# Performance work log

Hardware: AMD Instinct MI355X
Metric: run time of the kernel (lower is better)

The kernel has to match this reference:

```python
import jax, jax.numpy as jnp
import numpy as np

B, Hh, Ww, C = 4, 64, 64, 64


def setup_inputs() -> dict:
    key = jax.random.key(0)
    ks = jax.random.split(key, 5)
    scale = 1.0 / np.sqrt(C)
    return {
        "x": jax.random.normal(ks[0], (B, Hh, Ww, C), dtype=jnp.float32),
        "Wq": jax.random.normal(ks[1], (C, C), dtype=jnp.float32) * scale,
        "bq": jnp.zeros((C,), dtype=jnp.float32),
        "Wk": jax.random.normal(ks[2], (C, C), dtype=jnp.float32) * scale,
        "bk": jnp.zeros((C,), dtype=jnp.float32),
        "Wv": jax.random.normal(ks[3], (C, C), dtype=jnp.float32) * scale,
        "bv": jnp.zeros((C,), dtype=jnp.float32),
        "gamma": jax.random.normal(ks[4], (1,), dtype=jnp.float32) * 0.05,
    }


def reference(x, Wq, bq, Wk, bk, Wv, bv, gamma):
    b, h, w, c = x.shape
    n = h * w
    # 1x1 convs == per-pixel dense projections
    q = (jnp.einsum('bhwc,cf->bhwf', x, Wq) + bq).reshape(b, n, c)
    k = (jnp.einsum('bhwc,cf->bhwf', x, Wk) + bk).reshape(b, n, c)
    v = (jnp.einsum('bhwc,cf->bhwf', x, Wv) + bv).reshape(b, n, c)
    # energy[b, i, j] = <q_i, k_j>; no scaling, softmax over last axis (j)
    energy = jnp.einsum('bic,bjc->bij', q, k)
    attn = jax.nn.softmax(energy, axis=-1)
    # original: transpose(matmul(value^T, attention)) -> out[b,n,c] = sum_m attn[b,m,n] * v[b,m,c]
    out = jnp.einsum('bmn,bmc->bnc', attn, v)
    out = out.reshape(b, h, w, c)
    return gamma * out + x
```

## Files before the change

### kernel.cpp

```cpp
#include <hip/hip_runtime.h>
#include <hip/hip_bf16.h>


typedef __attribute__((ext_vector_type(8))) short short8;
typedef __attribute__((ext_vector_type(4))) short short4b;
typedef __attribute__((ext_vector_type(4))) float f32x4;
typedef __attribute__((ext_vector_type(4))) unsigned int u32x4;
typedef __attribute__((ext_vector_type(2))) unsigned int u32x2;

#define DEV static __device__ __forceinline__
#define LOG2E 1.4426950408889634f

DEV unsigned short f2bf(float f) {
    __hip_bfloat16 h = __float2bfloat16(f);
    return __builtin_bit_cast(unsigned short, h);
}
DEV unsigned int pack2(float lo, float hi) {
    return (unsigned int)f2bf(lo) | ((unsigned int)f2bf(hi) << 16);
}
DEV f32x4 MFMA32(short8 a, short8 b, f32x4 c) {
    return __builtin_amdgcn_mfma_f32_16x16x32_bf16(a, b, c, 0, 0, 0);
}
DEV f32x4 MFMA16(short4b a, short4b b, f32x4 c) {
#if __has_builtin(__builtin_amdgcn_mfma_f32_16x16x16_bf16)
    return __builtin_amdgcn_mfma_f32_16x16x16_bf16(a, b, c, 0, 0, 0);
#elif __has_builtin(__builtin_amdgcn_mfma_f32_16x16x16bf16_1k)
    return __builtin_amdgcn_mfma_f32_16x16x16bf16_1k(a, b, c, 0, 0, 0);
#else
    f32x4 d = c;
    asm volatile("v_mfma_f32_16x16x16_bf16 %0, %1, %2, %0" : "+v"(d) : "v"(a), "v"(b));
    return d;
#endif
}
DEV float EXP2(float x) {
#if __has_builtin(__builtin_amdgcn_exp2f)
    return __builtin_amdgcn_exp2f(x);
#else
    return exp2f(x);
#endif
}

#define OFF_Q    0u
#define OFF_K    2097152u
#define OFF_VT   4194304u
#define OFF_WT   6291456u
#define OFF_S    6316032u
#define OFF_LR   6381568u

__global__ __launch_bounds__(256) void k0z(const float* __restrict__ Wq,
                                           const float* __restrict__ Wk,
                                           const float* __restrict__ Wv,
                                           unsigned short* __restrict__ wt,
                                           float* __restrict__ sbuf) {
    int e = blockIdx.x * 256 + threadIdx.x;
    sbuf[e] = 0.0f;
    if (e < 3 * 4096) {
        int w3 = e >> 12, rem = e & 4095, f = rem >> 6, c = rem & 63;
        const float* W = (w3 == 0) ? Wq : (w3 == 1) ? Wk : Wv;
        float s = (w3 == 0) ? LOG2E : 1.0f;
        wt[e] = f2bf(W[c * 64 + f] * s);
    }
}

__global__ __launch_bounds__(256) void k1_proj(const float* __restrict__ x,
                                               const unsigned short* __restrict__ wt,
                                               const float* __restrict__ bq,
                                               const float* __restrict__ bk,
                                               const float* __restrict__ bv,
                                               unsigned short* __restrict__ qg,
                                               unsigned short* __restrict__ kg,
                                               unsigned short* __restrict__ vtg) {
    __shared__ __align__(16) char XT[8192];
    __shared__ __align__(16) char WT1[8192];
    __shared__ __align__(16) char VTILE[9216];
    int t = threadIdx.x, blk = blockIdx.x;
    int w3 = blk >> 8, rb = blk & 255;

    {
        int m = t >> 2, q4 = t & 3;
        const f32x4* xs = (const f32x4*)(x + (size_t)(rb * 64 + m) * 64 + q4 * 16);
        f32x4 fa = xs[0], f2 = xs[1], fc = xs[2], fd = xs[3];
        u32x4 u0 = { pack2(fa[0],fa[1]), pack2(fa[2],fa[3]), pack2(f2[0],f2[1]), pack2(f2[2],f2[3]) };
        u32x4 u1 = { pack2(fc[0],fc[1]), pack2(fc[2],fc[3]), pack2(fd[0],fd[1]), pack2(fd[2],fd[3]) };
        int sw = (m & 7) << 4;
        *(u32x4*)(XT + m * 128 + ((q4 * 32) ^ sw)) = u0;
        *(u32x4*)(XT + m * 128 + ((q4 * 32 + 16) ^ sw)) = u1;
    }
    {
        int f = t >> 2, q4 = t & 3;
        const u32x4* s = (const u32x4*)(wt + w3 * 4096 + f * 64 + q4 * 16);
        u32x4 u0 = s[0], u1 = s[1];
        int sw = (f & 7) << 4;
        *(u32x4*)(WT1 + f * 128 + ((q4 * 32) ^ sw)) = u0;
        *(u32x4*)(WT1 + f * 128 + ((q4 * 32 + 16) ^ sw)) = u1;
    }
    __syncthreads();

    int lane = t & 63, wid = t >> 6, g = lane >> 4, ln = lane & 15;
    int arow = wid * 16 + ln;
    short8 a0 = *(const short8*)(XT + arow * 128 + ((16 * g) ^ ((arow & 7) << 4)));
    short8 a1 = *(const short8*)(XT + arow * 128 + ((64 + 16 * g) ^ ((arow & 7) << 4)));
    const float* bias = (w3 == 0) ? bq : (w3 == 1) ? bk : bv;
    float bscale = (w3 == 0) ? LOG2E : 1.0f;

    #pragma unroll
    for (int fb = 0; fb < 4; ++fb) {
        int frow = fb * 16 + ln;
        short8 b0 = *(const short8*)(WT1 + frow * 128 + ((16 * g) ^ ((frow & 7) << 4)));
        short8 b1 = *(const short8*)(WT1 + frow * 128 + ((64 + 16 * g) ^ ((frow & 7) << 4)));
        f32x4 acc = {0.f, 0.f, 0.f, 0.f};
        acc = MFMA32(a0, b0, acc);
        acc = MFMA32(a1, b1, acc);
        float bval = bias[frow] * bscale;
        if (w3 < 2) {
            unsigned short* dst = (w3 == 0) ? qg : kg;
            int gr = rb * 64 + wid * 16 + 4 * g;
            #pragma unroll
            for (int r = 0; r < 4; ++r)
                dst[(size_t)(gr + r) * 64 + frow] = f2bf(acc[r] + bval);
        } else {
            unsigned short* vt = (unsigned short*)VTILE;
            int mloc = wid * 16 + 4 * g;
            #pragma unroll
            for (int r = 0; r < 4; ++r)
                vt[frow * 72 + mloc + r] = f2bf(acc[r] + bval);
        }
    }
    if (w3 == 2) {
        __syncthreads();
        int f = t >> 2, mq = t & 3;
        u32x4 u0 = *(const u32x4*)(VTILE + f * 144 + mq * 32);
        u32x4 u1 = *(const u32x4*)(VTILE + f * 144 + mq * 32 + 16);
        int b = rb >> 6, n0 = (rb & 63) * 64;
        unsigned short* dst = vtg + (size_t)b * 262144 + f * 4096 + n0 + mq * 16;
        *(u32x4*)(dst) = u0;
        *(u32x4*)(dst + 8) = u1;
    }
}

__global__ __launch_bounds__(256, 8) void k2_rowsum(const unsigned short* __restrict__ qg,
                                                    const unsigned short* __restrict__ kg,
                                                    float* __restrict__ sbuf) {
    __shared__ __align__(16) char QT[8192];
    __shared__ __align__(16) char KT2[2][4096];
    int t = threadIdx.x, blk = blockIdx.x;
    int b = blk >> 9, ns = (blk >> 6) & 7, mb = blk & 63;
    int m0 = mb * 64, nbase = ns * 512;

    {
        int row = t >> 2, q4 = t & 3, sw = (row & 7) << 4;
        const u32x4* s = (const u32x4*)(qg + (size_t)(b * 4096 + m0 + row) * 64 + q4 * 16);
        u32x4 u0 = s[0], u1 = s[1];
        *(u32x4*)(QT + row * 128 + ((q4 * 32) ^ sw)) = u0;
        *(u32x4*)(QT + row * 128 + ((q4 * 32 + 16) ^ sw)) = u1;
    }
    int srow = t >> 3, sb = t & 7, ssw = (srow & 7) << 4;
    const unsigned short* kbase = kg + (size_t)(b * 4096 + nbase) * 64;
    {
        u32x4 u = *(const u32x4*)(kbase + srow * 64 + sb * 8);
        *(u32x4*)(KT2[0] + srow * 128 + ((sb * 16) ^ ssw)) = u;
    }
    __syncthreads();

    int lane = t & 63, wid = t >> 6, g = lane >> 4, ln = lane & 15;
    int arow = wid * 16 + ln;
    short8 a0 = *(const short8*)(QT + arow * 128 + ((16 * g) ^ ((arow & 7) << 4)));
    short8 a1 = *(const short8*)(QT + arow * 128 + ((64 + 16 * g) ^ ((arow & 7) << 4)));

    float acc0 = 0.f, acc1 = 0.f, acc2 = 0.f, acc3 = 0.f;
    int buf = 0;
    u32x4 pf;
    for (int nc = 0; nc < 16; ++nc) {
        if (nc < 15)
            pf = *(const u32x4*)(kbase + (size_t)((nc + 1) * 32 + srow) * 64 + sb * 8);
        const char* kt = KT2[buf];
        #pragma unroll
        for (int j = 0; j < 2; ++j) {
            int brow = j * 16 + ln, bsw = (brow & 7) << 4;
            short8 kb0 = *(const short8*)(kt + brow * 128 + ((16 * g) ^ bsw));
            short8 kb1 = *(const short8*)(kt + brow * 128 + ((64 + 16 * g) ^ bsw));
            f32x4 e = {0.f, 0.f, 0.f, 0.f};
            e = MFMA32(a0, kb0, e);
            e = MFMA32(a1, kb1, e);
            acc0 += EXP2(e[0]); acc1 += EXP2(e[1]);
            acc2 += EXP2(e[2]); acc3 += EXP2(e[3]);
        }
        if (nc < 15)
            *(u32x4*)(KT2[buf ^ 1] + srow * 128 + ((sb * 16) ^ ssw)) = pf;
        __syncthreads();
        buf ^= 1;
    }
    #pragma unroll
    for (int msk = 1; msk < 16; msk <<= 1) {
        acc0 += __shfl_xor(acc0, msk);
        acc1 += __shfl_xor(acc1, msk);
        acc2 += __shfl_xor(acc2, msk);
        acc3 += __shfl_xor(acc3, msk);
    }
    if (ln == 0) {
        float* base = sbuf + b * 4096 + m0 + wid * 16 + 4 * g;
        unsafeAtomicAdd(base + 0, acc0);
        unsafeAtomicAdd(base + 1, acc1);
        unsafeAtomicAdd(base + 2, acc2);
        unsafeAtomicAdd(base + 3, acc3);
    }
}

__global__ __launch_bounds__(256) void r2_init(const float* __restrict__ sbuf,
                                               float* __restrict__ lrbuf,
                                               const float* __restrict__ x,
                                               float* __restrict__ outp) {
    int tid = blockIdx.x * 256 + threadIdx.x;
    if (tid < 16384) lrbuf[tid] = -__log2f(sbuf[tid]);
    f32x4 v = *(const f32x4*)(x + 4 * (size_t)tid);
    *(f32x4*)(outp + 4 * (size_t)tid) = v;
}

__global__ __launch_bounds__(256, 8) void k3_out(const unsigned short* __restrict__ qg,
                                                 const unsigned short* __restrict__ kg,
                                                 const unsigned short* __restrict__ vtg,
                                                 const float* __restrict__ lrbuf,
                                                 const float* __restrict__ gamma,
                                                 float* __restrict__ outp) {
    __shared__ __align__(16) char KT[8192];
    __shared__ __align__(16) char QT2[2][2048];
    __shared__ __align__(16) char VT2[2][2560];
    int t = threadIdx.x, blk = blockIdx.x;
    int b = blk >> 9, ms = (blk >> 6) & 7, nb = blk & 63;
    int n0 = nb * 64, mbase = ms * 512;

    {
        int row = t >> 2, q4 = t & 3, sw = (row & 7) << 4;
        const u32x4* s = (const u32x4*)(kg + (size_t)(b * 4096 + n0 + row) * 64 + q4 * 16);
        u32x4 u0 = s[0], u1 = s[1];
        *(u32x4*)(KT + row * 128 + ((q4 * 32) ^ sw)) = u0;
        *(u32x4*)(KT + row * 128 + ((q4 * 32 + 16) ^ sw)) = u1;
    }
    int qrow = t >> 4, qh = t & 15;
    int vc = t >> 2, vq = t & 3;
    int qssw = (qrow & 7) << 4;
    const unsigned short* qbase = qg + (size_t)(b * 4096 + mbase) * 64;
    const unsigned short* vbase = vtg + (size_t)b * 262144 + (size_t)vc * 4096 + mbase;
    {
        u32x2 qu = *(const u32x2*)(qbase + qrow * 64 + qh * 4);
        *(u32x2*)(QT2[0] + qrow * 128 + ((qh * 8) ^ qssw)) = qu;
        u32x2 vu = *(const u32x2*)(vbase + vq * 4);
        *(u32x2*)(VT2[0] + vc * 40 + vq * 8) = vu;
    }
    int lane = t & 63, wid = t >> 6, g = lane >> 4, ln = lane & 15;
    const float* lrb = lrbuf + b * 4096 + mbase + 4 * g;
    f32x4 lcur = *(const f32x4*)(lrb);
    __syncthreads();

    int krow = wid * 16 + ln, ksw = (krow & 7) << 4;
    short8 kb0 = *(const short8*)(KT + krow * 128 + ((16 * g) ^ ksw));
    short8 kb1 = *(const short8*)(KT + krow * 128 + ((64 + 16 * g) ^ ksw));

    f32x4 z = {0.f, 0.f, 0.f, 0.f};
    f32x4 oacc[4] = {z, z, z, z};
    int qsw = (ln & 7) << 4;
    int buf = 0;
    u32x2 qpf, vpf;
    f32x4 lnext;

    for (int mc = 0; mc < 32; ++mc) {
        if (mc < 31) {
            qpf = *(const u32x2*)(qbase + (size_t)((mc + 1) * 16 + qrow) * 64 + qh * 4);
            vpf = *(const u32x2*)(vbase + (mc + 1) * 16 + vq * 4);
            lnext = *(const f32x4*)(lrb + (mc + 1) * 16);
        }
        const char* qt = QT2[buf];
        const char* vt = VT2[buf];
        short8 as0 = *(const short8*)(qt + ln * 128 + ((16 * g) ^ qsw));
        short8 as1 = *(const short8*)(qt + ln * 128 + ((64 + 16 * g) ^ qsw));
        f32x4 e = MFMA32(as1, kb1, MFMA32(as0, kb0, lcur));
        float p0 = EXP2(e[0]), p1 = EXP2(e[1]), p2 = EXP2(e[2]), p3 = EXP2(e[3]);
        u32x2 pw = { pack2(p0, p1), pack2(p2, p3) };
        short4b pa = __builtin_bit_cast(short4b, pw);
        #pragma unroll
        for (int fb = 0; fb < 4; ++fb) {
            short4b vb = *(const short4b*)(vt + (fb * 16 + ln) * 40 + g * 8);
            oacc[fb] = MFMA16(pa, vb, oacc[fb]);
        }
        if (mc < 31) {
            *(u32x2*)(QT2[buf ^ 1] + qrow * 128 + ((qh * 8) ^ qssw)) = qpf;
            *(u32x2*)(VT2[buf ^ 1] + vc * 40 + vq * 8) = vpf;
            lcur = lnext;
        }
        __syncthreads();
        buf ^= 1;
    }

    float gm = gamma[0];
    int nr = b * 4096 + n0 + wid * 16 + 4 * g;
    #pragma unroll
    for (int fb = 0; fb < 4; ++fb) {
        #pragma unroll
        for (int r = 0; r < 4; ++r)
            unsafeAtomicAdd(outp + (size_t)(nr + r) * 64 + fb * 16 + ln, gm * oacc[fb][r]);
    }
}

extern "C" void kernel_launch(void* const* d_in, const int* in_sizes, int n_in,
                              void* d_out, int out_size, void* d_ws, size_t ws_size,
                              hipStream_t stream) {
    const float* x  = (const float*)d_in[0];
    const float* Wq = (const float*)d_in[1];
    const float* bq = (const float*)d_in[2];
    const float* Wk = (const float*)d_in[3];
    const float* bk = (const float*)d_in[4];
    const float* Wv = (const float*)d_in[5];
    const float* bv = (const float*)d_in[6];
    const float* gm = (const float*)d_in[7];
    char* ws = (char*)d_ws;
    float* outp = (float*)d_out;

    unsigned short* qg  = (unsigned short*)(ws + OFF_Q);
    unsigned short* kg  = (unsigned short*)(ws + OFF_K);
    unsigned short* vtg = (unsigned short*)(ws + OFF_VT);
    unsigned short* wt  = (unsigned short*)(ws + OFF_WT);
    float* sbuf         = (float*)(ws + OFF_S);
    float* lrbuf        = (float*)(ws + OFF_LR);

    k0z<<<64, 256, 0, stream>>>(Wq, Wk, Wv, wt, sbuf);
    k1_proj<<<768, 256, 0, stream>>>(x, wt, bq, bk, bv, qg, kg, vtg);
    k2_rowsum<<<2048, 256, 0, stream>>>(qg, kg, sbuf);
    r2_init<<<1024, 256, 0, stream>>>(sbuf, lrbuf, x, outp);
    k3_out<<<2048, 256, 0, stream>>>(qg, kg, vtg, lrbuf, gm, outp);
}
```

Measured before the change: 141.2 us.

## Load MFMA operands directly from global memory, dropping LDS staging and barriers

Both the rowsum and output kernels stop staging Q, K and V tiles in shared memory. Each lane now loads its MFMA fragments straight from global memory into registers, with register double-buffering and no __syncthreads in the loop. The output kernel also swaps bf16 round-to-nearest packing for plain truncation and lowers its launch_bounds occupancy hint from 8 to 6. This removes LDS traffic and barrier stalls, but relies on L1/L2 to serve the redundant per-wave loads and loses some precision in the attention weights.

```diff
diff --git a/kernel.cpp b/kernel.cpp
--- a/kernel.cpp
+++ b/kernel.cpp
@@ -17,6 +17,11 @@
 }
 DEV unsigned int pack2(float lo, float hi) {
     return (unsigned int)f2bf(lo) | ((unsigned int)f2bf(hi) << 16);
+}
+DEV unsigned int pack2t(float lo, float hi) {
+    unsigned int ul = __builtin_bit_cast(unsigned int, lo);
+    unsigned int uh = __builtin_bit_cast(unsigned int, hi);
+    return (uh & 0xffff0000u) | (ul >> 16);
 }
 DEV f32x4 MFMA32(short8 a, short8 b, f32x4 c) {
     return __builtin_amdgcn_mfma_f32_16x16x32_bf16(a, b, c, 0, 0, 0);
@@ -141,54 +146,32 @@
 __global__ __launch_bounds__(256, 8) void k2_rowsum(const unsigned short* __restrict__ qg,
                                                     const unsigned short* __restrict__ kg,
                                                     float* __restrict__ sbuf) {
-    __shared__ __align__(16) char QT[8192];
-    __shared__ __align__(16) char KT2[2][4096];
     int t = threadIdx.x, blk = blockIdx.x;
     int b = blk >> 9, ns = (blk >> 6) & 7, mb = blk & 63;
     int m0 = mb * 64, nbase = ns * 512;
-
-    {
-        int row = t >> 2, q4 = t & 3, sw = (row & 7) << 4;
-        const u32x4* s = (const u32x4*)(qg + (size_t)(b * 4096 + m0 + row) * 64 + q4 * 16);
-        u32x4 u0 = s[0], u1 = s[1];
-        *(u32x4*)(QT + row * 128 + ((q4 * 32) ^ sw)) = u0;
-        *(u32x4*)(QT + row * 128 + ((q4 * 32 + 16) ^ sw)) = u1;
-    }
-    int srow = t >> 3, sb = t & 7, ssw = (srow & 7) << 4;
-    const unsigned short* kbase = kg + (size_t)(b * 4096 + nbase) * 64;
-    {
-        u32x4 u = *(const u32x4*)(kbase + srow * 64 + sb * 8);
-        *(u32x4*)(KT2[0] + srow * 128 + ((sb * 16) ^ ssw)) = u;
-    }
-    __syncthreads();
-
     int lane = t & 63, wid = t >> 6, g = lane >> 4, ln = lane & 15;
-    int arow = wid * 16 + ln;
-    short8 a0 = *(const short8*)(QT + arow * 128 + ((16 * g) ^ ((arow & 7) << 4)));
-    short8 a1 = *(const short8*)(QT + arow * 128 + ((64 + 16 * g) ^ ((arow & 7) << 4)));
+
+    const unsigned short* qr = qg + (size_t)(b * 4096 + m0 + wid * 16 + ln) * 64;
+    short8 a0 = *(const short8*)(qr + 8 * g);
+    short8 a1 = *(const short8*)(qr + 32 + 8 * g);
+
+    const unsigned short* kbase = kg + (size_t)(b * 4096 + nbase + ln) * 64 + 8 * g;
+    short8 kb0 = *(const short8*)(kbase);
+    short8 kb1 = *(const short8*)(kbase + 32);
 
     float acc0 = 0.f, acc1 = 0.f, acc2 = 0.f, acc3 = 0.f;
-    int buf = 0;
-    u32x4 pf;
-    for (int nc = 0; nc < 16; ++nc) {
-        if (nc < 15)
-            pf = *(const u32x4*)(kbase + (size_t)((nc + 1) * 32 + srow) * 64 + sb * 8);
-        const char* kt = KT2[buf];
-        #pragma unroll
-        for (int j = 0; j < 2; ++j) {
-            int brow = j * 16 + ln, bsw = (brow & 7) << 4;
-            short8 kb0 = *(const short8*)(kt + brow * 128 + ((16 * g) ^ bsw));
-            short8 kb1 = *(const short8*)(kt + brow * 128 + ((64 + 16 * g) ^ bsw));
-            f32x4 e = {0.f, 0.f, 0.f, 0.f};
-            e = MFMA32(a0, kb0, e);
-            e = MFMA32(a1, kb1, e);
-            acc0 += EXP2(e[0]); acc1 += EXP2(e[1]);
-            acc2 += EXP2(e[2]); acc3 += EXP2(e[3]);
+    for (int s = 0; s < 32; ++s) {
+        short8 nb0, nb1;
+        if (s < 31) {
+            const unsigned short* kp = kbase + (size_t)(s + 1) * 16 * 64;
+            nb0 = *(const short8*)(kp);
+            nb1 = *(const short8*)(kp + 32);
         }
-        if (nc < 15)
-            *(u32x4*)(KT2[buf ^ 1] + srow * 128 + ((sb * 16) ^ ssw)) = pf;
-        __syncthreads();
-        buf ^= 1;
+        f32x4 z = {0.f, 0.f, 0.f, 0.f};
+        f32x4 e = MFMA32(a1, kb1, MFMA32(a0, kb0, z));
+        acc0 += EXP2(e[0]); acc1 += EXP2(e[1]);
+        acc2 += EXP2(e[2]); acc3 += EXP2(e[3]);
+        kb0 = nb0; kb1 = nb1;
     }
     #pragma unroll
     for (int msk = 1; msk < 16; msk <<= 1) {
@@ -216,79 +199,63 @@
     *(f32x4*)(outp + 4 * (size_t)tid) = v;
 }
 
-__global__ __launch_bounds__(256, 8) void k3_out(const unsigned short* __restrict__ qg,
+__global__ __launch_bounds__(256, 6) void k3_out(const unsigned short* __restrict__ qg,
                                                  const unsigned short* __restrict__ kg,
                                                  const unsigned short* __restrict__ vtg,
                                                  const float* __restrict__ lrbuf,
                                                  const float* __restrict__ gamma,
                                                  float* __restrict__ outp) {
-    __shared__ __align__(16) char KT[8192];
-    __shared__ __align__(16) char QT2[2][2048];
-    __shared__ __align__(16) char VT2[2][2560];
     int t = threadIdx.x, blk = blockIdx.x;
     int b = blk >> 9, ms = (blk >> 6) & 7, nb = blk & 63;
     int n0 = nb * 64, mbase = ms * 512;
-
-    {
-        int row = t >> 2, q4 = t & 3, sw = (row & 7) << 4;
-        const u32x4* s = (const u32x4*)(kg + (size_t)(b * 4096 + n0 + row) * 64 + q4 * 16);
-        u32x4 u0 = s[0], u1 = s[1];
-        *(u32x4*)(KT + row * 128 + ((q4 * 32) ^ sw)) = u0;
-        *(u32x4*)(KT + row * 128 + ((q4 * 32 + 16) ^ sw)) = u1;
-    }
-    int qrow = t >> 4, qh = t & 15;
-    int vc = t >> 2, vq = t & 3;
-    int qssw = (qrow & 7) << 4;
-    const unsigned short* qbase = qg + (size_t)(b * 4096 + mbase) * 64;
-    const unsigned short* vbase = vtg + (size_t)b * 262144 + (size_t)vc * 4096 + mbase;
-    {
-        u32x2 qu = *(const u32x2*)(qbase + qrow * 64 + qh * 4);
-        *(u32x2*)(QT2[0] + qrow * 128 + ((qh * 8) ^ qssw)) = qu;
-        u32x2 vu = *(const u32x2*)(vbase + vq * 4);
-        *(u32x2*)(VT2[0] + vc * 40 + vq * 8) = vu;
-    }
     int lane = t & 63, wid = t >> 6, g = lane >> 4, ln = lane & 15;
+
+    const unsigned short* krp = kg + (size_t)(b * 4096 + n0 + wid * 16 + ln) * 64;
+    short8 kb0 = *(const short8*)(krp + 8 * g);
+    short8 kb1 = *(const short8*)(krp + 32 + 8 * g);
+
+    const unsigned short* qbase = qg + (size_t)(b * 4096 + mbase + ln) * 64 + 8 * g;
+    const unsigned short* vtb = vtg + (size_t)b * 262144 + mbase;
     const float* lrb = lrbuf + b * 4096 + mbase + 4 * g;
+
+    short8 as0 = *(const short8*)(qbase);
+    short8 as1 = *(const short8*)(qbase + 32);
+    short4b vb0 = *(const short4b*)(vtb + (size_t)(ln) * 4096 + 4 * g);
+    short4b vb1 = *(const short4b*)(vtb + (size_t)(16 + ln) * 4096 + 4 * g);
+    short4b vb2 = *(const short4b*)(vtb + (size_t)(32 + ln) * 4096 + 4 * g);
+    short4b vb3 = *(const short4b*)(vtb + (size_t)(48 + ln) * 4096 + 4 * g);
     f32x4 lcur = *(const f32x4*)(lrb);
-    __syncthreads();
-
-    int krow = wid * 16 + ln, ksw = (krow & 7) << 4;
-    short8 kb0 = *(const short8*)(KT + krow * 128 + ((16 * g) ^ ksw));
-    short8 kb1 = *(const short8*)(KT + krow * 128 + ((64 + 16 * g) ^ ksw));
 
     f32x4 z = {0.f, 0.f, 0.f, 0.f};
     f32x4 oacc[4] = {z, z, z, z};
-    int qsw = (ln & 7) << 4;
-    int buf = 0;
-    u32x2 qpf, vpf;
-    f32x4 lnext;
 
     for (int mc = 0; mc < 32; ++mc) {
+        short8 nas0, nas1;
+        short4b nvb0, nvb1, nvb2, nvb3;
+        f32x4 lnext;
         if (mc < 31) {
-            qpf = *(const u32x2*)(qbase + (size_t)((mc + 1) * 16 + qrow) * 64 + qh * 4);
-            vpf = *(const u32x2*)(vbase + (mc + 1) * 16 + vq * 4);
-            lnext = *(const f32x4*)(lrb + (mc + 1) * 16);
+            int moff = (mc + 1) * 16;
+            const unsigned short* qp = qbase + (size_t)moff * 64;
+            nas0 = *(const short8*)(qp);
+            nas1 = *(const short8*)(qp + 32);
+            const unsigned short* vp = vtb + moff + 4 * g;
+            nvb0 = *(const short4b*)(vp + (size_t)(ln) * 4096);
+            nvb1 = *(const short4b*)(vp + (size_t)(16 + ln) * 4096);
+            nvb2 = *(const short4b*)(vp + (size_t)(32 + ln) * 4096);
+            nvb3 = *(const short4b*)(vp + (size_t)(48 + ln) * 4096);
+            lnext = *(const f32x4*)(lrb + moff);
         }
-        const char* qt = QT2[buf];
-        const char* vt = VT2[buf];
-        short8 as0 = *(const short8*)(qt + ln * 128 + ((16 * g) ^ qsw));
-        short8 as1 = *(const short8*)(qt + ln * 128 + ((64 + 16 * g) ^ qsw));
         f32x4 e = MFMA32(as1, kb1, MFMA32(as0, kb0, lcur));
         float p0 = EXP2(e[0]), p1 = EXP2(e[1]), p2 = EXP2(e[2]), p3 = EXP2(e[3]);
-        u32x2 pw = { pack2(p0, p1), pack2(p2, p3) };
+        u32x2 pw = { pack2t(p0, p1), pack2t(p2, p3) };
         short4b pa = __builtin_bit_cast(short4b, pw);
-        #pragma unroll
-        for (int fb = 0; fb < 4; ++fb) {
-            short4b vb = *(const short4b*)(vt + (fb * 16 + ln) * 40 + g * 8);
-            oacc[fb] = MFMA16(pa, vb, oacc[fb]);
-        }
-        if (mc < 31) {
-            *(u32x2*)(QT2[buf ^ 1] + qrow * 128 + ((qh * 8) ^ qssw)) = qpf;
-            *(u32x2*)(VT2[buf ^ 1] + vc * 40 + vq * 8) = vpf;
-            lcur = lnext;
-        }
-        __syncthreads();
-        buf ^= 1;
+        oacc[0] = MFMA16(pa, vb0, oacc[0]);
+        oacc[1] = MFMA16(pa, vb1, oacc[1]);
+        oacc[2] = MFMA16(pa, vb2, oacc[2]);
+        oacc[3] = MFMA16(pa, vb3, oacc[3]);
+        as0 = nas0; as1 = nas1;
+        vb0 = nvb0; vb1 = nvb1; vb2 = nvb2; vb3 = nvb3;
+        lcur = lnext;
     }
 
     float gm = gamma[0];
```

After: 321.2 us. 128% more time.
